# Kernel optimization log

Measured on AMD Instinct MI355X. Metric: run time of the kernel, lower is better.

## Reference

```python
import jax, jax.numpy as jnp
import numpy as np

N, K, D = 32768, 8192, 512
COMMITMENT_COST = 0.25

def setup_inputs() -> dict:
    key = jax.random.key(0)
    k1, k2 = jax.random.split(key)
    z = jax.random.normal(k1, (N, D), dtype=jnp.float32)
    # original inits uniform(-1/K, 1/K); scaled uniform keeps same distribution
    emb_weight = jax.random.uniform(k2, (K, D), dtype=jnp.float32, minval=-1.0 / K, maxval=1.0 / K)
    return {"z": z, "emb_weight": emb_weight}

def reference(z, emb_weight):
    z_flat = z.reshape(-1, emb_weight.shape[1])  # [N, D]
    # squared L2 distances: ||z||^2 + ||e||^2 - 2 z e^T  -> [N, K]
    distances = (
        jnp.sum(z_flat ** 2, axis=1, keepdims=True)
        + jnp.sum(emb_weight ** 2, axis=1)
        - 2.0 * jnp.matmul(z_flat, emb_weight.T)
    )
    code_indices = jnp.argmin(distances, axis=1)  # [N]
    quantized = emb_weight[code_indices]          # [N, D] gather
    e_latent_loss = jnp.mean((jax.lax.stop_gradient(quantized) - z_flat) ** 2)
    q_latent_loss = jnp.mean((quantized - jax.lax.stop_gradient(z_flat)) ** 2)
    loss = q_latent_loss + COMMITMENT_COST * e_latent_loss
    # straight-through estimator
    quantized_st = z_flat + jax.lax.stop_gradient(quantized - z_flat)
    return quantized_st, loss, code_indices
```

## Files before the change

### kernel.cpp

```cpp
#include <hip/hip_runtime.h>


#define N_ROWS 32768
#define K_CODES 8192
#define DIM 512

typedef __attribute__((ext_vector_type(8))) short short8;
typedef __attribute__((ext_vector_type(4))) float f32x4;

#define MARGIN 5e-4f

__device__ __forceinline__ unsigned short f2bf(float f) {
  unsigned int u = __float_as_uint(f);
  u = u + 0x7fffu + ((u >> 16) & 1u);
  return (unsigned short)(u >> 16);
}

__device__ __forceinline__ double shfl_xor_dbl(double v, int m) {
  union { double d; int i[2]; } u;
  u.d = v;
  u.i[0] = __shfl_xor(u.i[0], m, 64);
  u.i[1] = __shfl_xor(u.i[1], m, 64);
  return u.d;
}

__device__ __forceinline__ float opaque_f(float x) {
  asm volatile("" : "+v"(x));
  return x;
}

__global__ __launch_bounds__(256) void cvtnorm_k(const float* __restrict__ in,
                                                 unsigned short* __restrict__ outb,
                                                 float* __restrict__ outn) {
  const int r = blockIdx.x * 4 + (threadIdx.x >> 6);
  const int lane = threadIdx.x & 63;
  const float* xr = in + (size_t)r * DIM + lane * 8;
  const float4 a = *(const float4*)xr;
  const float4 b = *(const float4*)(xr + 4);
  uint4 o;
  o.x = (unsigned)f2bf(a.x) | ((unsigned)f2bf(a.y) << 16);
  o.y = (unsigned)f2bf(a.z) | ((unsigned)f2bf(a.w) << 16);
  o.z = (unsigned)f2bf(b.x) | ((unsigned)f2bf(b.y) << 16);
  o.w = (unsigned)f2bf(b.z) | ((unsigned)f2bf(b.w) << 16);
  *(uint4*)(outb + (size_t)r * DIM + lane * 8) = o;
  double s = (double)a.x * a.x + (double)a.y * a.y + (double)a.z * a.z + (double)a.w * a.w
           + (double)b.x * b.x + (double)b.y * b.y + (double)b.z * b.z + (double)b.w * b.w;
#pragma unroll
  for (int m = 1; m < 64; m <<= 1) s += shfl_xor_dbl(s, m);
  if (lane == 0) outn[r] = (float)s;
}

__global__ __launch_bounds__(512, 4) void gemm_topk(
    const unsigned short* __restrict__ A,
    const unsigned short* __restrict__ B,
    const float* __restrict__ en2,
    float* __restrict__ candk,
    int* __restrict__ candi)
{
  __shared__ char lds[77824];
  float* scorebuf = (float*)lds;
  float* e2sAll = (float*)(lds + 73728);

  const int tid = threadIdx.x;
  const int lane = tid & 63, wave = tid >> 6;
  const int wm = wave >> 1, wn = wave & 1;
  const int quad = lane >> 4, lcol = lane & 15;
  const int bx = blockIdx.x >> 3, by = blockIdx.x & 7;
  const int row0 = bx * 256;
  const int cstart = by * 1024;
  const int hf = tid & 1, srow = tid >> 1;

  e2sAll[tid] = en2[cstart + tid];
  e2sAll[tid + 512] = en2[cstart + 512 + tid];

  float tk0 = 3.4e38f, tk1 = 3.4e38f, tk2 = 3.4e38f, tk3 = 3.4e38f;
  int ti0 = 0, ti1 = 0, ti2 = 0, ti3 = 0;

  const int schm = (lane & 3) ^ ((lane >> 3) & 3);
  const unsigned short* Ag =
      A + ((size_t)(row0 + wave * 32 + (lane >> 2))) * DIM + schm * 8;
  const int dstA = wave * 2048;
  const int dstB = 16384 + wave * 1024;

  const int swz = (quad ^ ((lcol >> 1) & 3)) * 16;
  int aoff[4], boff[4];
#pragma unroll
  for (int i = 0; i < 4; ++i) aoff[i] = (wm * 64 + i * 16 + lcol) * 64 + swz;
#pragma unroll
  for (int j = 0; j < 4; ++j) boff[j] = 16384 + (wn * 64 + j * 16 + lcol) * 64 + swz;

#define ASGP const __attribute__((address_space(1))) void*
#define LDSP __attribute__((address_space(3))) void*
#define STAGE(ktv, bb) do {                                                        \
    const unsigned short* As_ = Ag + (ktv) * 32;                                   \
    const unsigned short* Bs_ = Bg + (ktv) * 32;                                   \
    __builtin_amdgcn_global_load_lds((ASGP)(uintptr_t)(As_),                       \
        (LDSP)(uintptr_t)(lds + (bb) + dstA), 16, 0, 0);                           \
    __builtin_amdgcn_global_load_lds((ASGP)(uintptr_t)(As_ + 16 * DIM),            \
        (LDSP)(uintptr_t)(lds + (bb) + dstA + 1024), 16, 0, 0);                    \
    __builtin_amdgcn_global_load_lds((ASGP)(uintptr_t)(Bs_),                       \
        (LDSP)(uintptr_t)(lds + (bb) + dstB), 16, 0, 0);                           \
  } while (0)

#define COMPUTE(cbb) do {                                                          \
    short8 af[4], bv[4];                                                           \
    _Pragma("unroll")                                                              \
    for (int i = 0; i < 4; ++i) af[i] = *(const short8*)(lds + (cbb) + aoff[i]);   \
    _Pragma("unroll")                                                              \
    for (int j = 0; j < 4; ++j) bv[j] = *(const short8*)(lds + (cbb) + boff[j]);   \
    _Pragma("unroll")                                                              \
    for (int i = 0; i < 4; ++i)                                                    \
      _Pragma("unroll")                                                            \
      for (int j = 0; j < 4; ++j)                                                  \
        acc[i][j] = __builtin_amdgcn_mfma_f32_16x16x32_bf16(af[i], bv[j],          \
                                                            acc[i][j], 0, 0, 0);   \
  } while (0)

#pragma unroll 1
  for (int ct = 0; ct < 8; ++ct) {
    const int c0 = cstart + ct * 128;
    const unsigned short* Bg =
        B + ((size_t)(c0 + wave * 16 + (lane >> 2))) * DIM + schm * 8;

    f32x4 acc[4][4];
#pragma unroll
    for (int i = 0; i < 4; ++i)
#pragma unroll
      for (int j = 0; j < 4; ++j) acc[i][j] = 0.f;

    __syncthreads();
    STAGE(0, 0);
    STAGE(1, 24576);
    int cb = 0, nb = 24576, fb = 49152;
#pragma unroll 1
    for (int kt = 0; kt < 15; ++kt) {
      asm volatile("s_waitcnt vmcnt(3)" ::: "memory");
      __builtin_amdgcn_s_barrier();
      asm volatile("" ::: "memory");
      __builtin_amdgcn_sched_barrier(0);
      if (kt < 14) STAGE(kt + 2, fb);
      COMPUTE(cb);
      const int t = cb; cb = nb; nb = fb; fb = t;
    }
    asm volatile("s_waitcnt vmcnt(0)" ::: "memory");
    __builtin_amdgcn_s_barrier();
    asm volatile("" ::: "memory");
    __builtin_amdgcn_sched_barrier(0);
    COMPUTE(cb);

#pragma unroll 1
    for (int h = 0; h < 2; ++h) {
      __syncthreads();
      if (wn == h) {
#pragma unroll
        for (int i = 0; i < 4; ++i)
#pragma unroll
          for (int j = 0; j < 4; ++j) {
            const float eb2 = e2sAll[ct * 128 + 64 * h + 16 * j + lcol];
#pragma unroll
            for (int r = 0; r < 4; ++r)
              scorebuf[(wm * 64 + i * 16 + quad * 4 + r) * 67 + 16 * j + lcol] =
                  fmaf(acc[i][j][r], -2.0f, eb2);
          }
      }
      __syncthreads();
      const float* sp = scorebuf + srow * 67 + hf * 32;
      const int idbase = c0 + 64 * h + 32 * hf;
#pragma unroll 8
      for (int cc = 0; cc < 32; ++cc) {
        const float key = sp[cc];
        if (key < tk3) {
          const int id = idbase + cc;
          if (key < tk2) {
            tk3 = tk2; ti3 = ti2;
            if (key < tk1) {
              tk2 = tk1; ti2 = ti1;
              if (key < tk0) { tk1 = tk0; ti1 = ti0; tk0 = key; ti0 = id; }
              else           { tk1 = key; ti1 = id; }
            } else { tk2 = key; ti2 = id; }
          } else { tk3 = key; ti3 = id; }
        }
      }
    }
  }

  const size_t cb2 = ((size_t)(row0 + srow)) * 64 + by * 8 + hf * 4;
  candk[cb2 + 0] = tk0; candk[cb2 + 1] = tk1; candk[cb2 + 2] = tk2; candk[cb2 + 3] = tk3;
  candi[cb2 + 0] = ti0; candi[cb2 + 1] = ti1; candi[cb2 + 2] = ti2; candi[cb2 + 3] = ti3;
}

__global__ __launch_bounds__(256) void rescore_np(
    const float* __restrict__ z, const float* __restrict__ e,
    const float* __restrict__ a32, const float* __restrict__ b32,
    const float* __restrict__ candk, const int* __restrict__ candi,
    float* __restrict__ idxout)
{
  const int row = blockIdx.x * 4 + (threadIdx.x >> 6);
  const int lane = threadIdx.x & 63;

  const float myk = candk[(size_t)row * 64 + lane];
  float kmin = myk;
#pragma unroll
  for (int m = 1; m < 64; m <<= 1) kmin = fminf(kmin, __shfl_xor(kmin, m, 64));
  const float cut = kmin + MARGIN;

  float bd = 3.4e38f;
  int bc = 0x7fffffff;
  if (myk <= cut) {
    const int c = candi[(size_t)row * 64 + lane];
    const float* zr = z + (size_t)row * DIM;
    const float* er = e + (size_t)c * DIM;
    float s = 0.0f;
#pragma unroll 4
    for (int k4 = 0; k4 < 96; ++k4) {
      const float4 zv = *(const float4*)(zr + k4 * 4);
      const float4 ev = *(const float4*)(er + k4 * 4);
      s = fmaf(zv.x, ev.x, s);
      s = fmaf(zv.y, ev.y, s);
      s = fmaf(zv.z, ev.z, s);
      s = fmaf(zv.w, ev.w, s);
    }
    const float cA = s;
    s = 0.0f;
#pragma unroll 4
    for (int k4 = 96; k4 < 128; ++k4) {
      const float4 zv = *(const float4*)(zr + k4 * 4);
      const float4 ev = *(const float4*)(er + k4 * 4);
      s = fmaf(zv.x, ev.x, s);
      s = fmaf(zv.y, ev.y, s);
      s = fmaf(zv.z, ev.z, s);
      s = fmaf(zv.w, ev.w, s);
    }
    const float m = cA + s;
    const float t1 = a32[row] + b32[c];
    const float t2 = opaque_f(2.0f * m);
    bd = t1 - t2;
    bc = c;
  }
#pragma unroll
  for (int mm = 1; mm < 64; mm <<= 1) {
    const float od = __shfl_xor(bd, mm, 64);
    const int oc = __shfl_xor(bc, mm, 64);
    if (od < bd || (od == bd && oc < bc)) { bd = od; bc = oc; }
  }
  if (lane == 0) idxout[row] = (float)bc;
}

__global__ __launch_bounds__(256) void writeout_k(
    const float* __restrict__ z, const float* __restrict__ e,
    const float* __restrict__ idxf, float* __restrict__ outq,
    double* __restrict__ accum)
{
  const int tid = threadIdx.x;
  double s = 0.0;
  size_t gid = (size_t)blockIdx.x * 256 + tid;
#pragma unroll 1
  for (int it = 0; it < 16; ++it, gid += 262144) {
    const int row = (int)(gid >> 7);
    const int dq = ((int)gid & 127) << 2;
    const int c = (int)idxf[row];
    const float4 q4 = *(const float4*)(e + (size_t)c * DIM + dq);
    const float4 z4 = *(const float4*)(z + (size_t)row * DIM + dq);
    const float tx = q4.x - z4.x, ty = q4.y - z4.y, tz = q4.z - z4.z, tw = q4.w - z4.w;
    float4 o;
    o.x = z4.x + tx; o.y = z4.y + ty; o.z = z4.z + tz; o.w = z4.w + tw;
    *(float4*)(outq + (size_t)row * DIM + dq) = o;
    s += (double)tx * tx + (double)ty * ty + (double)tz * tz + (double)tw * tw;
  }
#pragma unroll
  for (int m = 1; m < 64; m <<= 1) s += shfl_xor_dbl(s, m);
  __shared__ double wsum[4];
  if ((tid & 63) == 0) wsum[tid >> 6] = s;
  __syncthreads();
  if (tid == 0) atomicAdd(accum, wsum[0] + wsum[1] + wsum[2] + wsum[3]);
}

__global__ void finalize_k(const double* __restrict__ accum, float* __restrict__ lossp) {
  *lossp = (float)(1.25 * accum[0] / (double)((size_t)N_ROWS * DIM));
}

extern "C" void kernel_launch(void* const* d_in, const int* in_sizes, int n_in,
                              void* d_out, int out_size, void* d_ws, size_t ws_size,
                              hipStream_t stream) {
  const float* z = (const float*)d_in[0];
  const float* e = (const float*)d_in[1];
  float* out = (float*)d_out;
  char* ob = (char*)d_out;

  unsigned short* zb = (unsigned short*)ob;
  unsigned short* eb = (unsigned short*)(ob + 33554432);
  float* b32   = (float*)(ob + 41943040);
  float* a32   = (float*)(ob + 41975808);
  float* candk = (float*)(ob + 42106880);
  int*   candi = (int*)(ob + 50495488);

  float* lossp = out + 16777216;
  float* idxs  = out + 16777217;
  double* accum = (double*)d_ws;

  hipMemsetAsync(d_ws, 0, sizeof(double), stream);
  cvtnorm_k<<<8192, 256, 0, stream>>>(z, zb, a32);
  cvtnorm_k<<<2048, 256, 0, stream>>>(e, eb, b32);
  gemm_topk<<<1024, 512, 0, stream>>>(zb, eb, b32, candk, candi);
  rescore_np<<<8192, 256, 0, stream>>>(z, e, a32, b32, candk, candi, idxs);
  writeout_k<<<1024, 256, 0, stream>>>(z, e, idxs, out, accum);
  finalize_k<<<1, 1, 0, stream>>>(accum, lossp);
}
```

Measured before the change: 788.2 us.

## Do top-4 selection directly from MFMA accumulators in registers, drop LDS score staging

Swaps the MFMA operand order so each lane's accumulator holds four consecutive codes for a single row. The per-lane top-4 is then kept in registers straight from the accumulators, and the per-row lists are merged across quads with wave shuffles. This removes the LDS score buffer write/read round trip and the two extra block barriers per code tile. In exchange it uses many more registers (16 top-k slots per lane) and adds shuffle-merge work, which may lower occupancy under the 512-thread launch bounds.

```diff
diff --git a/kernel.cpp b/kernel.cpp
--- a/kernel.cpp
+++ b/kernel.cpp
@@ -50,6 +50,51 @@
   if (lane == 0) outn[r] = (float)s;
 }
 
+
+#define DECL_TOPK(J) \
+  float tk##J##0 = 3.4e38f, tk##J##1 = 3.4e38f, tk##J##2 = 3.4e38f, tk##J##3 = 3.4e38f; \
+  int ti##J##0 = 0, ti##J##1 = 0, ti##J##2 = 0, ti##J##3 = 0;
+
+#define INS(J, sv, idv) do { \
+    if ((sv) < tk##J##3) { \
+      if ((sv) < tk##J##2) { tk##J##3 = tk##J##2; ti##J##3 = ti##J##2; \
+        if ((sv) < tk##J##1) { tk##J##2 = tk##J##1; ti##J##2 = ti##J##1; \
+          if ((sv) < tk##J##0) { tk##J##1 = tk##J##0; ti##J##1 = ti##J##0; tk##J##0 = (sv); ti##J##0 = (idv); } \
+          else { tk##J##1 = (sv); ti##J##1 = (idv); } \
+        } else { tk##J##2 = (sv); ti##J##2 = (idv); } \
+      } else { tk##J##3 = (sv); ti##J##3 = (idv); } \
+    } \
+  } while (0)
+
+#define LTL(sv, idv, K, I) ((sv) < (K) || ((sv) == (K) && (idv) < (I)))
+#define INSM(J, sv, idv) do { \
+    if (LTL(sv, idv, tk##J##3, ti##J##3)) { \
+      if (LTL(sv, idv, tk##J##2, ti##J##2)) { tk##J##3 = tk##J##2; ti##J##3 = ti##J##2; \
+        if (LTL(sv, idv, tk##J##1, ti##J##1)) { tk##J##2 = tk##J##1; ti##J##2 = ti##J##1; \
+          if (LTL(sv, idv, tk##J##0, ti##J##0)) { tk##J##1 = tk##J##0; ti##J##1 = ti##J##0; tk##J##0 = (sv); ti##J##0 = (idv); } \
+          else { tk##J##1 = (sv); ti##J##1 = (idv); } \
+        } else { tk##J##2 = (sv); ti##J##2 = (idv); } \
+      } else { tk##J##3 = (sv); ti##J##3 = (idv); } \
+    } \
+  } while (0)
+
+#define SCAN_J(J) do { \
+    float s0_ = fmaf(acc[i][J][0], -2.0f, e0), s1_ = fmaf(acc[i][J][1], -2.0f, e1); \
+    float s2_ = fmaf(acc[i][J][2], -2.0f, e2v), s3_ = fmaf(acc[i][J][3], -2.0f, e3); \
+    const float mn_ = fminf(fminf(s0_, s1_), fminf(s2_, s3_)); \
+    if (mn_ < tk##J##3) { \
+      INS(J, s0_, id0); INS(J, s1_, id0 + 1); INS(J, s2_, id0 + 2); INS(J, s3_, id0 + 3); \
+    } \
+  } while (0)
+
+#define MERGE_STEP(J, M) do { \
+    float ok0 = __shfl_xor(tk##J##0, M, 64), ok1 = __shfl_xor(tk##J##1, M, 64); \
+    float ok2 = __shfl_xor(tk##J##2, M, 64), ok3 = __shfl_xor(tk##J##3, M, 64); \
+    int oi0 = __shfl_xor(ti##J##0, M, 64), oi1 = __shfl_xor(ti##J##1, M, 64); \
+    int oi2 = __shfl_xor(ti##J##2, M, 64), oi3 = __shfl_xor(ti##J##3, M, 64); \
+    INSM(J, ok0, oi0); INSM(J, ok1, oi1); INSM(J, ok2, oi2); INSM(J, ok3, oi3); \
+  } while (0)
+
 __global__ __launch_bounds__(512, 4) void gemm_topk(
     const unsigned short* __restrict__ A,
     const unsigned short* __restrict__ B,
@@ -58,7 +103,6 @@
     int* __restrict__ candi)
 {
   __shared__ char lds[77824];
-  float* scorebuf = (float*)lds;
   float* e2sAll = (float*)(lds + 73728);
 
   const int tid = threadIdx.x;
@@ -68,13 +112,11 @@
   const int bx = blockIdx.x >> 3, by = blockIdx.x & 7;
   const int row0 = bx * 256;
   const int cstart = by * 1024;
-  const int hf = tid & 1, srow = tid >> 1;
 
   e2sAll[tid] = en2[cstart + tid];
   e2sAll[tid + 512] = en2[cstart + 512 + tid];
 
-  float tk0 = 3.4e38f, tk1 = 3.4e38f, tk2 = 3.4e38f, tk3 = 3.4e38f;
-  int ti0 = 0, ti1 = 0, ti2 = 0, ti3 = 0;
+  DECL_TOPK(0) DECL_TOPK(1) DECL_TOPK(2) DECL_TOPK(3)
 
   const int schm = (lane & 3) ^ ((lane >> 3) & 3);
   const unsigned short* Ag =
@@ -112,7 +154,7 @@
     for (int i = 0; i < 4; ++i)                                                    \
       _Pragma("unroll")                                                            \
       for (int j = 0; j < 4; ++j)                                                  \
-        acc[i][j] = __builtin_amdgcn_mfma_f32_16x16x32_bf16(af[i], bv[j],          \
+        acc[i][j] = __builtin_amdgcn_mfma_f32_16x16x32_bf16(bv[i], af[j],          \
                                                             acc[i][j], 0, 0, 0);   \
   } while (0)
 
@@ -148,45 +190,28 @@
     __builtin_amdgcn_sched_barrier(0);
     COMPUTE(cb);
 
-#pragma unroll 1
-    for (int h = 0; h < 2; ++h) {
-      __syncthreads();
-      if (wn == h) {
-#pragma unroll
-        for (int i = 0; i < 4; ++i)
-#pragma unroll
-          for (int j = 0; j < 4; ++j) {
-            const float eb2 = e2sAll[ct * 128 + 64 * h + 16 * j + lcol];
-#pragma unroll
-            for (int r = 0; r < 4; ++r)
-              scorebuf[(wm * 64 + i * 16 + quad * 4 + r) * 67 + 16 * j + lcol] =
-                  fmaf(acc[i][j][r], -2.0f, eb2);
-          }
-      }
-      __syncthreads();
-      const float* sp = scorebuf + srow * 67 + hf * 32;
-      const int idbase = c0 + 64 * h + 32 * hf;
-#pragma unroll 8
-      for (int cc = 0; cc < 32; ++cc) {
-        const float key = sp[cc];
-        if (key < tk3) {
-          const int id = idbase + cc;
-          if (key < tk2) {
-            tk3 = tk2; ti3 = ti2;
-            if (key < tk1) {
-              tk2 = tk1; ti2 = ti1;
-              if (key < tk0) { tk1 = tk0; ti1 = ti0; tk0 = key; ti0 = id; }
-              else           { tk1 = key; ti1 = id; }
-            } else { tk2 = key; ti2 = id; }
-          } else { tk3 = key; ti3 = id; }
-        }
-      }
+#pragma unroll
+    for (int i = 0; i < 4; ++i) {
+      const int eb = ct * 128 + wn * 64 + i * 16 + quad * 4;
+      const float e0 = e2sAll[eb], e1 = e2sAll[eb + 1];
+      const float e2v = e2sAll[eb + 2], e3 = e2sAll[eb + 3];
+      const int id0 = cstart + eb;
+      SCAN_J(0); SCAN_J(1); SCAN_J(2); SCAN_J(3);
     }
   }
 
-  const size_t cb2 = ((size_t)(row0 + srow)) * 64 + by * 8 + hf * 4;
-  candk[cb2 + 0] = tk0; candk[cb2 + 1] = tk1; candk[cb2 + 2] = tk2; candk[cb2 + 3] = tk3;
-  candi[cb2 + 0] = ti0; candi[cb2 + 1] = ti1; candi[cb2 + 2] = ti2; candi[cb2 + 3] = ti3;
+  MERGE_STEP(0, 16); MERGE_STEP(1, 16); MERGE_STEP(2, 16); MERGE_STEP(3, 16);
+  MERGE_STEP(0, 32); MERGE_STEP(1, 32); MERGE_STEP(2, 32); MERGE_STEP(3, 32);
+
+  if (quad == 0) {
+#define WOUT(J) do { \
+      const size_t cb2 = ((size_t)(row0 + wm * 64 + (J) * 16 + lcol)) * 64 + by * 8 + wn * 4; \
+      float4 kf; kf.x = tk##J##0; kf.y = tk##J##1; kf.z = tk##J##2; kf.w = tk##J##3; \
+      int4 fi; fi.x = ti##J##0; fi.y = ti##J##1; fi.z = ti##J##2; fi.w = ti##J##3; \
+      *(float4*)(candk + cb2) = kf; *(int4*)(candi + cb2) = fi; \
+    } while (0)
+    WOUT(0); WOUT(1); WOUT(2); WOUT(3);
+  }
 }
 
 __global__ __launch_bounds__(256) void rescore_np(
```

After: 827.3 us. 1.05x slower.
